# Optimization experiments

Measured on AMD Instinct MI355X. Metric: run time of the kernel, lower is better.

Reference implementation:

```python
import jax, jax.numpy as jnp
import numpy as np
from jax import lax


def setup_inputs() -> dict:
    key = jax.random.key(0)
    k1, k2 = jax.random.split(key)
    N, D_IN, D_MODEL, ORDER_K = 8192, 1024, 1024, 8
    scale = 1.0 / np.sqrt(D_IN)
    x = jax.random.normal(k1, (N, D_IN), dtype=jnp.float32)
    weights = jax.random.normal(k2, (ORDER_K + 1, D_IN, D_MODEL), dtype=jnp.float32) * scale
    return {"x": x, "weights": weights}


def reference(x, weights):
    # x: [N, d_in]; weights: [K+1, d_in, d_model]
    x32 = x.astype(jnp.float32)
    t0 = jnp.ones_like(x32)                      # T_0(x) = 1
    out = t0 @ weights[0] + x32 @ weights[1]     # T_0 W_0 + T_1 W_1

    def step(carry, w_k):
        prev2, prev1, acc = carry
        tk = 2.0 * x32 * prev1 - prev2           # Chebyshev recurrence T_k
        acc = acc + tk @ w_k
        return (prev1, tk, acc), None

    (_, _, out), _ = lax.scan(step, (t0, x32, out), weights[2:])
    return out
```

## Files before the change

### kernel.cpp

```cpp
#include <hip/hip_runtime.h>
#include <hip/hip_bf16.h>
#include <stdint.h>

typedef float  f32x4 __attribute__((ext_vector_type(4)));
typedef short  s16x8 __attribute__((ext_vector_type(8)));

#define GLOAD_LDS16(g, l)                                                          \
  __builtin_amdgcn_global_load_lds(                                               \
      (const __attribute__((address_space(1))) unsigned int*)(g),                 \
      (__attribute__((address_space(3))) unsigned int*)(l), 16, 0, 0)

#define WAITVM_(N) asm volatile("s_waitcnt vmcnt(" #N ")" ::: "memory")
#define WAITVM(N) WAITVM_(N)
#define WAITLGKM0 asm volatile("s_waitcnt lgkmcnt(0)" ::: "memory")

static __device__ __forceinline__ unsigned short f2bf(float f) {
  union { __hip_bfloat16 b; unsigned short s; } cv;
  cv.b = __float2bfloat16(f);
  return cv.s;
}

static __device__ __forceinline__ int swz_e(int r) { return ((r & 3) ^ ((r >> 2) & 1)); }
static __device__ __forceinline__ int swz_byte(int r, int c) {
  return r * 64 + (((c ^ swz_e(r)) & 3) << 4);
}

__global__ __launch_bounds__(256) void transpose_w(const float* __restrict__ w,
                                                   short* __restrict__ wt) {
  __shared__ unsigned int lds[64 * 33];
  const int t = threadIdx.x;
  const int bid = blockIdx.x;
  const int kb = bid >> 8;
  const int db = (bid >> 4) & 15;
  const int cb = bid & 15;
  const int d0 = db * 64, c0 = cb * 64;
  const float* src = w + (size_t)(kb + 1) * 1048576 + (size_t)d0 * 1024 + c0;
  #pragma unroll
  for (int p = 0; p < 4; ++p) {
    int dl = p * 16 + (t >> 4);
    int c4 = (t & 15) * 4;
    f32x4 f = *(const f32x4*)(src + (size_t)dl * 1024 + c4);
    unsigned lo = (unsigned)f2bf(f.x) | ((unsigned)f2bf(f.y) << 16);
    unsigned hi = (unsigned)f2bf(f.z) | ((unsigned)f2bf(f.w) << 16);
    lds[dl * 33 + (t & 15) * 2]     = lo;
    lds[dl * 33 + (t & 15) * 2 + 1] = hi;
  }
  __syncthreads();
  const int col = t >> 2;
  const int dc  = t & 3;
  union { unsigned short u[8]; s16x8 v; } o0, o1;
  #pragma unroll
  for (int j = 0; j < 16; ++j) {
    int dl = dc * 16 + j;
    unsigned word = lds[dl * 33 + (col >> 1)];
    unsigned short e = (col & 1) ? (unsigned short)(word >> 16) : (unsigned short)(word & 0xffffu);
    if (j < 8) o0.u[j] = e; else o1.u[j - 8] = e;
  }
  short* dst = wt + ((size_t)(kb * 1024 + c0 + col) * 1024 + d0 + dc * 16);
  *(s16x8*)dst       = o0.v;
  *(s16x8*)(dst + 8) = o1.v;
}

__global__ __launch_bounds__(256) void bias_k(const float* __restrict__ w,
                                              float* __restrict__ b) {
  __shared__ float red[256];
  const int t = threadIdx.x;
  const int col = blockIdx.x * 64 + (t & 63);
  const int seg = t >> 6;
  float s = 0.f;
  const float* p = w + (size_t)(seg * 256) * 1024 + col;
  for (int d = 0; d < 256; ++d) s += p[(size_t)d * 1024];
  red[t] = s;
  __syncthreads();
  if (t < 64) b[col] = red[t] + red[t + 64] + red[t + 128] + red[t + 192];
}

__global__ __launch_bounds__(256) void init_out(const float* __restrict__ bias,
                                                float* __restrict__ out, int has_bias) {
  const size_t i = (size_t)blockIdx.x * 256 + threadIdx.x;
  const int c = (int)((i * 4) & 1023);
  f32x4 v = has_bias ? *(const f32x4*)(bias + c) : (f32x4){0.f, 0.f, 0.f, 0.f};
  *(f32x4*)(out + i * 4) = v;
}

template <bool USE_WS>
__global__ __launch_bounds__(256, 2) void cheb_gemm(
    const float* __restrict__ x, const float* __restrict__ w,
    const short* __restrict__ wt, float* __restrict__ out) {
  __shared__ short Asm[2][4096];
  __shared__ short Bsm[3][8192];

  const int tid = threadIdx.x, lane = tid & 63, wid = tid >> 6;
  const int bid = blockIdx.x;
  const int xcd = bid & 7;
  const int mb  = bid >> 3;
  const int nb  = xcd >> 1, kb = xcd & 1;
  const int rowbase = mb * 128, colbase = nb * 256;
  const int kbase = kb * 512;
  const int wr = wid >> 1, wc = wid & 1;
  const int la = lane & 15, lg = lane >> 4;

  f32x4 acc[4][8];
  #pragma unroll
  for (int m = 0; m < 4; ++m)
    #pragma unroll
    for (int n = 0; n < 8; ++n) acc[m][n] = (f32x4){0.f, 0.f, 0.f, 0.f};

  const int e_la = (la & 3) ^ ((la >> 2) & 1);
  const int abase = (wr * 64 + la) * 64 + ((lg ^ e_la) << 4);
  const int bbase = (wc * 128 + la) * 64 + ((lg ^ e_la) << 4);

  const int arow = tid & 127, h = tid >> 7;
  const int aw0 = swz_byte(arow, 2 * h), aw1 = swz_byte(arow, 2 * h + 1);
  const float* xrow = x + (size_t)(rowbase + arow) * 1024 + kbase + h * 16;

  float p1[16], p2[16];
  unsigned x2h[8];
  f32x4 xq[4];

  if constexpr (USE_WS) {
    const int bcol0  = wid * 64 + (lane >> 2);
    const int goff   = ((lane & 3) ^ swz_e(lane >> 2)) * 8;
    const short* gptr = wt + (size_t)(colbase + bcol0) * 1024 + kbase + goff;

#define ISSUE_AT(PTR, WOFF)                                                        \
    { _Pragma("unroll")                                                            \
      for (int j_ = 0; j_ < 4; ++j_)                                               \
        GLOAD_LDS16((PTR) + j_ * 16384,                                            \
                    (char*)&Bsm[0][0] + (WOFF) + (wid * 4 + j_) * 1024); }

    #pragma unroll
    for (int q = 0; q < 4; ++q) xq[q] = *(const f32x4*)(xrow + q * 4);
    ISSUE_AT(gptr, 0);          gptr += 1048576;
    ISSUE_AT(gptr, 16384);      gptr += 1048576;
    {
      union { unsigned short u[8]; s16x8 v; } o0, o1;
      #pragma unroll
      for (int i = 0; i < 16; ++i) { p1[i] = xq[i >> 2][i & 3]; p2[i] = 1.f; }
      #pragma unroll
      for (int i = 0; i < 8; ++i) {
        union { unsigned u; _Float16 f[2]; } t2;
        t2.f[0] = (_Float16)(p1[2 * i] + p1[2 * i]);
        t2.f[1] = (_Float16)(p1[2 * i + 1] + p1[2 * i + 1]);
        x2h[i] = t2.u;
        o0.u[i] = f2bf(p1[i]); o1.u[i] = f2bf(p1[i + 8]);
      }
      *(s16x8*)((char*)&Asm[0][0] + aw0) = o0.v;
      *(s16x8*)((char*)&Asm[0][0] + aw1) = o1.v;
    }
    WAITLGKM0;
    WAITVM(4);
    __builtin_amdgcn_sched_barrier(0);
    __builtin_amdgcn_s_barrier();
    __builtin_amdgcn_sched_barrier(0);

    int wroff = 32768;
    int rdoff = 0;
    int ard   = 0;

    #pragma unroll 1
    for (int t = 0; t < 128; ++t) {
      if ((t & 7) == 2 && t < 120) {
        const float* xs = xrow + ((t >> 3) + 1) * 32;
        #pragma unroll
        for (int q = 0; q < 4; ++q) xq[q] = *(const f32x4*)(xs + q * 4);
      }
      if (t + 2 < 128) {
        ISSUE_AT(gptr, wroff);
        gptr += ((t & 7) == 5) ? (32 - 7 * 1048576) : 1048576;
        wroff = (wroff == 32768) ? 0 : wroff + 16384;
      }
      if (t + 1 < 128) {
        const int rn = (t + 1) & 7;
        union { unsigned short u[8]; s16x8 v; } o0, o1;
        if (rn == 0) {
          #pragma unroll
          for (int i = 0; i < 16; ++i) { p1[i] = xq[i >> 2][i & 3]; p2[i] = 1.f; }
          #pragma unroll
          for (int i = 0; i < 8; ++i) {
            union { unsigned u; _Float16 f[2]; } t2;
            t2.f[0] = (_Float16)(p1[2 * i] + p1[2 * i]);
            t2.f[1] = (_Float16)(p1[2 * i + 1] + p1[2 * i + 1]);
            x2h[i] = t2.u;
            o0.u[i] = f2bf(p1[i]); o1.u[i] = f2bf(p1[i + 8]);
          }
        } else {
          #pragma unroll
          for (int i = 0; i < 16; ++i) {
            union { unsigned u; _Float16 f[2]; } t2; t2.u = x2h[i >> 1];
            float cur = fmaf((float)t2.f[i & 1], p1[i], -p2[i]);
            p2[i] = p1[i]; p1[i] = cur;
            unsigned short e = f2bf(cur);
            if (i < 8) o0.u[i] = e; else o1.u[i - 8] = e;
          }
        }
        *(s16x8*)((char*)&Asm[0][0] + (ard ^ 8192) + aw0) = o0.v;
        *(s16x8*)((char*)&Asm[0][0] + (ard ^ 8192) + aw1) = o1.v;
      }
      s16x8 af[4];
      #pragma unroll
      for (int m = 0; m < 4; ++m)
        af[m] = *(const s16x8*)((char*)&Asm[0][0] + ard + abase + m * 1024);
      __builtin_amdgcn_s_setprio(1);
      #pragma unroll
      for (int n = 0; n < 8; ++n) {
        s16x8 bfr = *(const s16x8*)((char*)&Bsm[0][0] + rdoff + bbase + n * 1024);
        #pragma unroll
        for (int m = 0; m < 4; ++m)
          acc[m][n] = __builtin_amdgcn_mfma_f32_16x16x32_bf16(af[m], bfr, acc[m][n], 0, 0, 0);
      }
      __builtin_amdgcn_s_setprio(0);
      WAITLGKM0;
      if (t < 126) { WAITVM(4); } else { WAITVM(0); }
      __builtin_amdgcn_sched_barrier(0);
      __builtin_amdgcn_s_barrier();
      __builtin_amdgcn_sched_barrier(0);
      rdoff = (rdoff == 32768) ? 0 : rdoff + 16384;
      ard ^= 8192;
    }
#undef ISSUE_AT
  } else {
    #pragma unroll 1
    for (int s = 0; s < 144; ++s) {
      const int r = s % 9, st = s / 9;
      const int d0 = kbase + st * 32;
      __syncthreads();
      { const int dd = tid & 31, cg = tid >> 5;
        const float* ws_ = w + (size_t)r * 1048576 + (size_t)(d0 + dd) * 1024 + colbase + cg * 4;
        #pragma unroll
        for (int p_ = 0; p_ < 8; ++p_) {
          f32x4 f_ = *(const f32x4*)(ws_ + p_ * 32);
          #pragma unroll
          for (int jj = 0; jj < 4; ++jj) {
            int col = cg * 4 + p_ * 32 + jj;
            int byt = col * 64 + ((dd & 7) << 1) + ((((dd >> 3) ^ swz_e(col)) & 3) << 4);
            *(unsigned short*)((char*)&Bsm[0][0] + byt) = f2bf(f_[jj]);
          } } }
      union { unsigned short u[8]; s16x8 v; } o0, o1;
      if (r == 0) {
        #pragma unroll
        for (int q = 0; q < 4; ++q) xq[q] = *(const f32x4*)(xrow + st * 32 + q * 4);
        #pragma unroll
        for (int i = 0; i < 16; ++i) { p1[i] = xq[i >> 2][i & 3]; p2[i] = 1.f; }
        #pragma unroll
        for (int i = 0; i < 8; ++i) {
          union { unsigned u; _Float16 f[2]; } t2;
          t2.f[0] = (_Float16)(p1[2 * i] + p1[2 * i]);
          t2.f[1] = (_Float16)(p1[2 * i + 1] + p1[2 * i + 1]);
          x2h[i] = t2.u;
          o0.u[i] = 0x3f80; o1.u[i] = 0x3f80;
        }
      } else if (r == 1) {
        #pragma unroll
        for (int i = 0; i < 8; ++i) { o0.u[i] = f2bf(p1[i]); o1.u[i] = f2bf(p1[i + 8]); }
      } else {
        #pragma unroll
        for (int i = 0; i < 16; ++i) {
          union { unsigned u; _Float16 f[2]; } t2; t2.u = x2h[i >> 1];
          float cur = fmaf((float)t2.f[i & 1], p1[i], -p2[i]);
          p2[i] = p1[i]; p1[i] = cur;
          if (i < 8) o0.u[i] = f2bf(cur); else o1.u[i - 8] = f2bf(cur);
        }
      }
      *(s16x8*)((char*)&Asm[0][0] + aw0) = o0.v;
      *(s16x8*)((char*)&Asm[0][0] + aw1) = o1.v;
      __syncthreads();
      s16x8 af[4];
      #pragma unroll
      for (int m = 0; m < 4; ++m)
        af[m] = *(const s16x8*)((char*)&Asm[0][0] + abase + m * 1024);
      #pragma unroll
      for (int n = 0; n < 8; ++n) {
        s16x8 bfr = *(const s16x8*)((char*)&Bsm[0][0] + bbase + n * 1024);
        #pragma unroll
        for (int m = 0; m < 4; ++m)
          acc[m][n] = __builtin_amdgcn_mfma_f32_16x16x32_bf16(af[m], bfr, acc[m][n], 0, 0, 0);
      }
    }
  }

  #pragma unroll
  for (int m = 0; m < 4; ++m) {
    const int r0 = rowbase + wr * 64 + m * 16 + lg * 4;
    #pragma unroll
    for (int n = 0; n < 8; ++n) {
      const int c = colbase + wc * 128 + n * 16 + la;
      #pragma unroll
      for (int j = 0; j < 4; ++j)
        unsafeAtomicAdd(&out[(size_t)(r0 + j) * 1024 + c], acc[m][n][j]);
    }
  }
}

extern "C" void kernel_launch(void* const* d_in, const int* in_sizes, int n_in,
                              void* d_out, int out_size, void* d_ws, size_t ws_size,
                              hipStream_t stream) {
  const float* x = (const float*)d_in[0];
  const float* w = (const float*)d_in[1];
  float* out = (float*)d_out;

  const size_t WT_BYTES = (size_t)8 * 1024 * 1024 * 2;
  const bool use_ws = ws_size >= WT_BYTES + 4096;

  if (use_ws) {
    short* wt   = (short*)d_ws;
    float* bias = (float*)((char*)d_ws + WT_BYTES);
    transpose_w<<<2048, 256, 0, stream>>>(w, wt);
    bias_k<<<16, 256, 0, stream>>>(w, bias);
    init_out<<<8192, 256, 0, stream>>>(bias, out, 1);
    cheb_gemm<true><<<512, 256, 0, stream>>>(x, w, wt, out);
  } else {
    init_out<<<8192, 256, 0, stream>>>(nullptr, out, 0);
    cheb_gemm<false><<<512, 256, 0, stream>>>(x, w, nullptr, out);
  }
}
```

Before: 214.1 us.

## Precompute Chebyshev A matrix in workspace and run one large-K bf16 GEMM

Result: slower. 250.6 us (+17.0%).

```diff
diff --git a/kernel.cpp b/kernel.cpp
--- a/kernel.cpp
+++ b/kernel.cpp
@@ -2,8 +2,8 @@
 #include <hip/hip_bf16.h>
 #include <stdint.h>
 
-typedef float  f32x4 __attribute__((ext_vector_type(4)));
-typedef short  s16x8 __attribute__((ext_vector_type(8)));
+typedef float  f32x4  __attribute__((ext_vector_type(4)));
+typedef short  s16x8  __attribute__((ext_vector_type(8)));
 
 #define GLOAD_LDS16(g, l)                                                          \
   __builtin_amdgcn_global_load_lds(                                               \
@@ -25,9 +25,75 @@
   return r * 64 + (((c ^ swz_e(r)) & 3) << 4);
 }
 
+__global__ __launch_bounds__(256) void agen(const float* __restrict__ x,
+                                            short* __restrict__ amat) {
+  const int g = blockIdx.x * 256 + threadIdx.x;
+  const int row = g >> 7;
+  const int d0 = (g & 127) << 3;
+  const float* xp = x + (size_t)row * 1024 + d0;
+  f32x4 a = *(const f32x4*)xp, b = *(const f32x4*)(xp + 4);
+  float p1[8], p2[8], x2[8];
+  #pragma unroll
+  for (int i = 0; i < 8; ++i) {
+    float v = (i < 4) ? a[i] : b[i - 4];
+    p1[i] = v; p2[i] = 1.f; x2[i] = v + v;
+  }
+  short* dst = amat + (size_t)row * 8192 + d0;
+  #pragma unroll
+  for (int k = 1; k <= 8; ++k) {
+    union { unsigned short u[8]; s16x8 v; } o;
+    #pragma unroll
+    for (int i = 0; i < 8; ++i) o.u[i] = f2bf(p1[i]);
+    *(s16x8*)(dst + (size_t)(k - 1) * 1024) = o.v;
+    if (k < 8) {
+      #pragma unroll
+      for (int i = 0; i < 8; ++i) {
+        float c = fmaf(x2[i], p1[i], -p2[i]);
+        p2[i] = p1[i]; p1[i] = c;
+      }
+    }
+  }
+}
+
+__global__ __launch_bounds__(256) void transpose_w2(const float* __restrict__ w,
+                                                    short* __restrict__ wt) {
+  __shared__ unsigned int ldsT[64 * 33];
+  const int t = threadIdx.x;
+  const int bid = blockIdx.x;
+  const int kk = bid >> 8;
+  const int db = (bid >> 4) & 15;
+  const int cb = bid & 15;
+  const int d0 = db * 64, c0 = cb * 64;
+  const float* src = w + (size_t)(kk + 1) * 1048576 + (size_t)d0 * 1024 + c0;
+  #pragma unroll
+  for (int p = 0; p < 4; ++p) {
+    int dl = p * 16 + (t >> 4);
+    int c4 = (t & 15) * 4;
+    f32x4 f = *(const f32x4*)(src + (size_t)dl * 1024 + c4);
+    unsigned lo = (unsigned)f2bf(f.x) | ((unsigned)f2bf(f.y) << 16);
+    unsigned hi = (unsigned)f2bf(f.z) | ((unsigned)f2bf(f.w) << 16);
+    ldsT[dl * 33 + (t & 15) * 2]     = lo;
+    ldsT[dl * 33 + (t & 15) * 2 + 1] = hi;
+  }
+  __syncthreads();
+  const int col = t >> 2;
+  const int dc  = t & 3;
+  union { unsigned short u[8]; s16x8 v; } o0, o1;
+  #pragma unroll
+  for (int j = 0; j < 16; ++j) {
+    int dl = dc * 16 + j;
+    unsigned word = ldsT[dl * 33 + (col >> 1)];
+    unsigned short e = (col & 1) ? (unsigned short)(word >> 16) : (unsigned short)(word & 0xffffu);
+    if (j < 8) o0.u[j] = e; else o1.u[j - 8] = e;
+  }
+  short* dst = wt + (size_t)(c0 + col) * 8192 + (size_t)kk * 1024 + d0 + dc * 16;
+  *(s16x8*)dst       = o0.v;
+  *(s16x8*)(dst + 8) = o1.v;
+}
+
 __global__ __launch_bounds__(256) void transpose_w(const float* __restrict__ w,
                                                    short* __restrict__ wt) {
-  __shared__ unsigned int lds[64 * 33];
+  __shared__ unsigned int ldsT[64 * 33];
   const int t = threadIdx.x;
   const int bid = blockIdx.x;
   const int kb = bid >> 8;
@@ -42,8 +108,8 @@
     f32x4 f = *(const f32x4*)(src + (size_t)dl * 1024 + c4);
     unsigned lo = (unsigned)f2bf(f.x) | ((unsigned)f2bf(f.y) << 16);
     unsigned hi = (unsigned)f2bf(f.z) | ((unsigned)f2bf(f.w) << 16);
-    lds[dl * 33 + (t & 15) * 2]     = lo;
-    lds[dl * 33 + (t & 15) * 2 + 1] = hi;
+    ldsT[dl * 33 + (t & 15) * 2]     = lo;
+    ldsT[dl * 33 + (t & 15) * 2 + 1] = hi;
   }
   __syncthreads();
   const int col = t >> 2;
@@ -52,7 +118,7 @@
   #pragma unroll
   for (int j = 0; j < 16; ++j) {
     int dl = dc * 16 + j;
-    unsigned word = lds[dl * 33 + (col >> 1)];
+    unsigned word = ldsT[dl * 33 + (col >> 1)];
     unsigned short e = (col & 1) ? (unsigned short)(word >> 16) : (unsigned short)(word & 0xffffu);
     if (j < 8) o0.u[j] = e; else o1.u[j - 8] = e;
   }
@@ -83,6 +149,117 @@
   *(f32x4*)(out + i * 4) = v;
 }
 
+__global__ __launch_bounds__(512, 2) void gemm8(
+    const short* __restrict__ amat, const short* __restrict__ wt2,
+    float* __restrict__ out) {
+  __shared__ __attribute__((aligned(16))) char lds[131072];
+
+  const int tid = threadIdx.x, lane = tid & 63, wid = tid >> 6;
+  const int bid = blockIdx.x;
+  const int xcd = bid & 7, mb = bid >> 3;
+  const int nb = xcd >> 1, kb = xcd & 1;
+  const int rowbase = mb * 256, colbase = nb * 256;
+  const int wr = wid >> 2, wc = wid & 3;
+  const int la = lane & 15, lg = lane >> 4;
+  const int ela = (la & 3) ^ ((la >> 2) & 1);
+
+  int aoff[4], boff[4];
+  #pragma unroll
+  for (int mm = 0; mm < 4; ++mm)
+    aoff[mm] = ((wr * 128 + mm * 16 + la) << 6) + ((lg ^ ela) << 4);
+  #pragma unroll
+  for (int n = 0; n < 4; ++n)
+    boff[n] = 65536 + ((wc * 64 + n * 16 + la) << 6) + ((lg ^ ela) << 4);
+
+  const int rr   = lane >> 2;
+  const int goff = ((lane & 3) ^ ((rr & 3) ^ ((rr >> 2) & 1))) * 8;
+  const int r0 = wid * 32 + rr, r1 = r0 + 16;
+  const size_t kk0 = (size_t)kb * 4096;
+  const short* asrc0 = amat + (size_t)(rowbase + r0) * 8192 + kk0 + goff;
+  const short* asrc1 = amat + (size_t)(rowbase + r1) * 8192 + kk0 + goff;
+  const short* bsrc0 = wt2 + (size_t)(colbase + r0) * 8192 + kk0 + goff;
+  const short* bsrc1 = wt2 + (size_t)(colbase + r1) * 8192 + kk0 + goff;
+  const int adst0 = wid * 2048, adst1 = adst0 + 1024;
+
+  f32x4 acc[8][4];
+  #pragma unroll
+  for (int m = 0; m < 8; ++m)
+    #pragma unroll
+    for (int n = 0; n < 4; ++n) acc[m][n] = (f32x4){0.f, 0.f, 0.f, 0.f};
+
+#define STAGE_A(T, SOFF)                                                           \
+  { GLOAD_LDS16(asrc0 + (T) * 32, lds + (SOFF) + adst0);                           \
+    GLOAD_LDS16(asrc1 + (T) * 32, lds + (SOFF) + adst1); }
+#define STAGE_B(T, SOFF)                                                           \
+  { GLOAD_LDS16(bsrc0 + (T) * 32, lds + 65536 + (SOFF) + adst0);                   \
+    GLOAD_LDS16(bsrc1 + (T) * 32, lds + 65536 + (SOFF) + adst1); }
+
+  STAGE_A(0, 0);     STAGE_B(0, 0);
+  STAGE_A(1, 16384); STAGE_B(1, 16384);
+  WAITVM(4);
+  __builtin_amdgcn_sched_barrier(0);
+  __builtin_amdgcn_s_barrier();
+  __builtin_amdgcn_sched_barrier(0);
+
+  #pragma unroll 1
+  for (int t = 0; t < 128; ++t) {
+    const int soff = (t & 3) << 14;
+    const int s2   = ((t + 2) & 3) << 14;
+    s16x8 bf[4], af[4];
+
+    #pragma unroll
+    for (int n = 0; n < 4; ++n) bf[n] = *(const s16x8*)(lds + soff + boff[n]);
+    #pragma unroll
+    for (int mm = 0; mm < 4; ++mm) af[mm] = *(const s16x8*)(lds + soff + aoff[mm]);
+    if (t + 2 < 128) STAGE_A(t + 2, s2);
+    __builtin_amdgcn_s_barrier();
+    WAITLGKM0;
+    __builtin_amdgcn_sched_barrier(0);
+    __builtin_amdgcn_s_setprio(1);
+    #pragma unroll
+    for (int n = 0; n < 4; ++n)
+      #pragma unroll
+      for (int mm = 0; mm < 4; ++mm)
+        acc[mm][n] = __builtin_amdgcn_mfma_f32_16x16x32_bf16(af[mm], bf[n], acc[mm][n], 0, 0, 0);
+    __builtin_amdgcn_s_setprio(0);
+    __builtin_amdgcn_sched_barrier(0);
+    __builtin_amdgcn_s_barrier();
+    __builtin_amdgcn_sched_barrier(0);
+
+    #pragma unroll
+    for (int mm = 0; mm < 4; ++mm) af[mm] = *(const s16x8*)(lds + soff + 4096 + aoff[mm]);
+    if (t + 2 < 128) STAGE_B(t + 2, s2);
+    __builtin_amdgcn_s_barrier();
+    WAITLGKM0;
+    __builtin_amdgcn_sched_barrier(0);
+    __builtin_amdgcn_s_setprio(1);
+    #pragma unroll
+    for (int n = 0; n < 4; ++n)
+      #pragma unroll
+      for (int mm = 0; mm < 4; ++mm)
+        acc[4 + mm][n] = __builtin_amdgcn_mfma_f32_16x16x32_bf16(af[mm], bf[n], acc[4 + mm][n], 0, 0, 0);
+    __builtin_amdgcn_s_setprio(0);
+    if (t < 126) { WAITVM(4); } else { WAITVM(0); }
+    __builtin_amdgcn_sched_barrier(0);
+    __builtin_amdgcn_s_barrier();
+    __builtin_amdgcn_sched_barrier(0);
+  }
+#undef STAGE_A
+#undef STAGE_B
+
+  #pragma unroll
+  for (int m = 0; m < 8; ++m) {
+    const int r0o = rowbase + wr * 128 + m * 16 + lg * 4;
+    #pragma unroll
+    for (int n = 0; n < 4; ++n) {
+      const int c = colbase + wc * 64 + n * 16 + la;
+      #pragma unroll
+      for (int j = 0; j < 4; ++j)
+        unsafeAtomicAdd(&out[(size_t)(r0o + j) * 1024 + c], acc[m][n][j]);
+    }
+  }
+}
+
 template <bool USE_WS>
 __global__ __launch_bounds__(256, 2) void cheb_gemm(
     const float* __restrict__ x, const float* __restrict__ w,
@@ -99,13 +276,6 @@
   const int kbase = kb * 512;
   const int wr = wid >> 1, wc = wid & 1;
   const int la = lane & 15, lg = lane >> 4;
-
-  f32x4 acc[4][8];
-  #pragma unroll
-  for (int m = 0; m < 4; ++m)
-    #pragma unroll
-    for (int n = 0; n < 8; ++n) acc[m][n] = (f32x4){0.f, 0.f, 0.f, 0.f};
-
   const int e_la = (la & 3) ^ ((la >> 2) & 1);
   const int abase = (wr * 64 + la) * 64 + ((lg ^ e_la) << 4);
   const int bbase = (wc * 128 + la) * 64 + ((lg ^ e_la) << 4);
@@ -117,6 +287,11 @@
   float p1[16], p2[16];
   unsigned x2h[8];
   f32x4 xq[4];
+  f32x4 acc[4][8];
+  #pragma unroll
+  for (int m = 0; m < 4; ++m)
+    #pragma unroll
+    for (int n = 0; n < 8; ++n) acc[m][n] = (f32x4){0.f, 0.f, 0.f, 0.f};
 
   if constexpr (USE_WS) {
     const int bcol0  = wid * 64 + (lane >> 2);
@@ -154,9 +329,7 @@
     __builtin_amdgcn_s_barrier();
     __builtin_amdgcn_sched_barrier(0);
 
-    int wroff = 32768;
-    int rdoff = 0;
-    int ard   = 0;
+    int wroff = 32768, rdoff = 0, ard = 0;
 
     #pragma unroll 1
     for (int t = 0; t < 128; ++t) {
@@ -201,7 +374,6 @@
       #pragma unroll
       for (int m = 0; m < 4; ++m)
         af[m] = *(const s16x8*)((char*)&Asm[0][0] + ard + abase + m * 1024);
-      __builtin_amdgcn_s_setprio(1);
       #pragma unroll
       for (int n = 0; n < 8; ++n) {
         s16x8 bfr = *(const s16x8*)((char*)&Bsm[0][0] + rdoff + bbase + n * 1024);
@@ -209,7 +381,6 @@
         for (int m = 0; m < 4; ++m)
           acc[m][n] = __builtin_amdgcn_mfma_f32_16x16x32_bf16(af[m], bfr, acc[m][n], 0, 0, 0);
       }
-      __builtin_amdgcn_s_setprio(0);
       WAITLGKM0;
       if (t < 126) { WAITVM(4); } else { WAITVM(0); }
       __builtin_amdgcn_sched_barrier(0);
@@ -299,10 +470,20 @@
   const float* w = (const float*)d_in[1];
   float* out = (float*)d_out;
 
-  const size_t WT_BYTES = (size_t)8 * 1024 * 1024 * 2;
-  const bool use_ws = ws_size >= WT_BYTES + 4096;
-
-  if (use_ws) {
+  const size_t AMAT_BYTES = (size_t)8192 * 8192 * 2;
+  const size_t WT2_BYTES  = (size_t)1024 * 8192 * 2;
+  const size_t WT_BYTES   = (size_t)8 * 1024 * 1024 * 2;
+
+  if (ws_size >= AMAT_BYTES + WT2_BYTES + 4096) {
+    short* amat = (short*)d_ws;
+    short* wt2  = (short*)((char*)d_ws + AMAT_BYTES);
+    float* bias = (float*)((char*)d_ws + AMAT_BYTES + WT2_BYTES);
+    agen<<<4096, 256, 0, stream>>>(x, amat);
+    transpose_w2<<<2048, 256, 0, stream>>>(w, wt2);
+    bias_k<<<16, 256, 0, stream>>>(w, bias);
+    init_out<<<8192, 256, 0, stream>>>(bias, out, 1);
+    gemm8<<<256, 512, 0, stream>>>(amat, wt2, out);
+  } else if (ws_size >= WT_BYTES + 4096) {
     short* wt   = (short*)d_ws;
     float* bias = (float*)((char*)d_ws + WT_BYTES);
     transpose_w<<<2048, 256, 0, stream>>>(w, wt);
```
